# Performance work log

Hardware: AMD Instinct MI355X
Metric: run time of the kernel (lower is better)

Reference implementation:

```python
import jax, jax.numpy as jnp
import numpy as np

B, D, N_NEG, MAX_N = 4096, 256, 32768, 16
NEG_INF = float(jnp.finfo(jnp.float32).min)

def _l2norm(x):
    return x / jnp.linalg.norm(x, axis=-1, keepdims=True)

def setup_inputs() -> dict:
    key = jax.random.key(0)
    kq, kp, kn = jax.random.split(key, 3)
    q_emb = _l2norm(jax.random.normal(kq, (B, D), dtype=jnp.float32))
    p_emb = _l2norm(jax.random.normal(kp, (B, D), dtype=jnp.float32))
    n_emb = _l2norm(jax.random.normal(kn, (N_NEG, D), dtype=jnp.float32))
    # ragged counts in [0,16], mean 8, summing exactly to N_NEG
    rng = np.random.default_rng(0)
    d = rng.integers(0, 9, size=B // 2)
    counts = np.concatenate([8 + d, 8 - d])
    rng.shuffle(counts)
    n_counts = jnp.asarray(counts, dtype=jnp.int32)
    log_tau = jnp.log(jnp.asarray(0.07, dtype=jnp.float32))
    return {"q_emb": q_emb, "p_emb": p_emb, "n_emb": n_emb,
            "n_counts": n_counts, "log_tau": log_tau}

def reference(q_emb, p_emb, n_emb, n_counts, log_tau):
    Bq = q_emb.shape[0]
    tau = jnp.clip(jnp.exp(log_tau), 1e-4, 1.0)
    sim = (q_emb @ p_emb.T) / tau                      # [B, B]
    n_sim = (q_emb @ n_emb.T) / tau                    # [B, N]
    # vectorized ragged packing: query i's negatives live at
    # n_sim[i, offset[i] : offset[i]+cnt[i]]
    offsets = jnp.cumsum(n_counts) - n_counts          # [B]
    col = offsets[:, None] + jnp.arange(MAX_N)[None, :]
    valid = jnp.arange(MAX_N)[None, :] < n_counts[:, None]
    gathered = jnp.take_along_axis(n_sim, jnp.clip(col, 0, n_sim.shape[1] - 1), axis=1)
    neg_cols = jnp.where(valid, gathered, NEG_INF)     # [B, MAX_N]
    full = jnp.concatenate([sim, neg_cols], axis=1)    # [B, B+MAX_N]
    labels = jnp.arange(Bq)
    logp_q = jax.nn.log_softmax(full, axis=-1)
    loss_q = -jnp.mean(jnp.take_along_axis(logp_q, labels[:, None], axis=1))
    logp_p = jax.nn.log_softmax(sim.T, axis=-1)
    loss_p = -jnp.mean(jnp.take_along_axis(logp_p, labels[:, None], axis=1))
    return (loss_q + loss_p) / 2.0
```

## Files before the change

kernel.cpp:

```cpp
#include <hip/hip_runtime.h>
#include <math.h>

#define BQ 4096
#define DD 256
#define NNEG 32768

typedef __bf16 bf16x8 __attribute__((ext_vector_type(8)));
typedef float f32x4 __attribute__((ext_vector_type(4)));

typedef const __attribute__((address_space(1))) void GvPtr;
typedef __attribute__((address_space(3))) void LdsPtr;


__device__ __forceinline__ float get_inv_tau(const float* __restrict__ lt) {
  float tau = __expf(lt[0]);
  tau = fminf(fmaxf(tau, 1e-4f), 1.0f);
  return 1.0f / tau;
}

__device__ __forceinline__ unsigned int f2bf(float f) {
  unsigned int u = __float_as_uint(f);
  u += 0x7FFFu + ((u >> 16) & 1u);
  return u >> 16;
}

__global__ __launch_bounds__(256) void prep_kernel(
    const float* __restrict__ q, const float* __restrict__ p,
    const int* __restrict__ counts,
    ushort* __restrict__ qb, ushort* __restrict__ pb,
    int* __restrict__ owner, float* __restrict__ rowcol ) {
  __shared__ int wtot[4];
  const int t = threadIdx.x;
  if (blockIdx.x < 1024) {
    const int i = blockIdx.x * 256 + t;
    const int half = (BQ * DD) / 8;
    const float* src = (i < half) ? q : p;
    ushort* dst = (i < half) ? qb : pb;
    const int idx = (i < half) ? i : (i - half);
    const float4 a = *reinterpret_cast<const float4*>(&src[idx * 8]);
    const float4 b = *reinterpret_cast<const float4*>(&src[idx * 8 + 4]);
    uint4 o;
    o.x = f2bf(a.x) | (f2bf(a.y) << 16);
    o.y = f2bf(a.z) | (f2bf(a.w) << 16);
    o.z = f2bf(b.x) | (f2bf(b.y) << 16);
    o.w = f2bf(b.z) | (f2bf(b.w) << 16);
    *reinterpret_cast<uint4*>(&dst[idx * 8]) = o;
    return;
  }
  const int wid = t >> 6, lane = t & 63;
  const float4 z = {0.f, 0.f, 0.f, 0.f};
#pragma unroll
  for (int i = 0; i < 8; ++i) reinterpret_cast<float4*>(rowcol)[t * 8 + i] = z;

  int cl[16];
  int s = 0;
#pragma unroll
  for (int i = 0; i < 4; ++i) {
    const int4 c = reinterpret_cast<const int4*>(counts)[t * 4 + i];
    cl[4 * i + 0] = c.x; cl[4 * i + 1] = c.y; cl[4 * i + 2] = c.z; cl[4 * i + 3] = c.w;
    s += c.x + c.y + c.z + c.w;
  }
  int x = s;
#pragma unroll
  for (int off = 1; off < 64; off <<= 1) {
    const int v = __shfl_up(x, off);
    if (lane >= off) x += v;
  }
  if (lane == 63) wtot[wid] = x;
  __syncthreads();
  int base = 0;
  for (int w = 0; w < wid; ++w) base += wtot[w];
  int running = base + x - s;
#pragma unroll
  for (int k = 0; k < 16; ++k) {
    const int qi = 16 * t + k;
    for (int e = 0; e < cl[k]; ++e) owner[running + e] = qi;
    running += cl[k];
  }
}

__global__ __launch_bounds__(256) void main_kernel(
    const ushort* __restrict__ qb, const ushort* __restrict__ pb,
    const float* __restrict__ q, const float* __restrict__ n_emb,
    const int* __restrict__ owner, const float* __restrict__ logtau,
    float* __restrict__ row_sum, float* __restrict__ col_sum,
    float* __restrict__ diag) {
  __shared__ ushort As[2][128 * 32];
  __shared__ ushort Bs[2][128 * 32];

  const int tid = threadIdx.x;
  const int bid = (int)blockIdx.x;
  const float inv_tau = get_inv_tau(logtau);

  const int lane = tid & 63;
  const int wv = tid >> 6;
  const int wr = wv >> 1, wc = wv & 1;
  const int lrow = lane >> 4;
  const int lcol = lane & 15;

  const int swz = (bid & 7) * 128 + (bid >> 3);
  const int bx = swz & 31, by = swz >> 5;
  const int brow = by * 128, bcol = bx * 128;

  const int sr = tid >> 2;
  const int sc = (tid & 3) * 8;

  f32x4 acc[4][4];
#pragma unroll
  for (int i = 0; i < 4; ++i)
#pragma unroll
    for (int j = 0; j < 4; ++j) acc[i][j] = (f32x4){0.f, 0.f, 0.f, 0.f};

#define STAGE(buf, k0)                                                          \
  {                                                                             \
    _Pragma("unroll")                                                           \
    for (int i = 0; i < 2; ++i) {                                               \
      const ushort* ga = qb + (size_t)(brow + i * 64 + sr) * DD + (k0) + sc;    \
      __builtin_amdgcn_global_load_lds((GvPtr*)ga,                              \
          (LdsPtr*)(&As[buf][0] + i * 2048 + tid * 8), 16, 0, 0);               \
      const ushort* gb = pb + (size_t)(bcol + i * 64 + sr) * DD + (k0) + sc;    \
      __builtin_amdgcn_global_load_lds((GvPtr*)gb,                              \
          (LdsPtr*)(&Bs[buf][0] + i * 2048 + tid * 8), 16, 0, 0);               \
    }                                                                           \
  }

  STAGE(0, 0);
  __syncthreads();

#pragma unroll
  for (int t = 0; t < 8; ++t) {
    if (t < 7) STAGE((t + 1) & 1, (t + 1) * 32);
    const ushort* lA = &As[t & 1][0];
    const ushort* lB = &Bs[t & 1][0];
    bf16x8 a[4], b[4];
#pragma unroll
    for (int m = 0; m < 4; ++m)
      a[m] = *reinterpret_cast<const bf16x8*>(lA + (wr * 64 + m * 16 + lcol) * 32 + lrow * 8);
#pragma unroll
    for (int n = 0; n < 4; ++n)
      b[n] = *reinterpret_cast<const bf16x8*>(lB + (wc * 64 + n * 16 + lcol) * 32 + lrow * 8);
#pragma unroll
    for (int m = 0; m < 4; ++m)
#pragma unroll
      for (int n = 0; n < 4; ++n)
        acc[m][n] = __builtin_amdgcn_mfma_f32_16x16x32_bf16(a[m], b[n], acc[m][n], 0, 0, 0);
    __syncthreads();
  }
#undef STAGE

  const int arow0 = brow + wr * 64;
  const int bcol0 = bcol + wc * 64;
  float colp[4] = {0.f, 0.f, 0.f, 0.f};
#pragma unroll
  for (int mi = 0; mi < 4; ++mi) {
    float rowp[4] = {0.f, 0.f, 0.f, 0.f};
#pragma unroll
    for (int ni = 0; ni < 4; ++ni) {
      const f32x4 v = acc[mi][ni];
#pragma unroll
      for (int r = 0; r < 4; ++r) {
        const float sv = v[r] * inv_tau;
        const float e = __expf(sv);
        const int gr = arow0 + mi * 16 + lrow * 4 + r;
        const int gc = bcol0 + ni * 16 + lcol;
        if (gr == gc) diag[gr] = sv;
        rowp[r] += e;
        colp[ni] += e;
      }
    }
#pragma unroll
    for (int r = 0; r < 4; ++r) {
      float x = rowp[r];
      x += __shfl_xor(x, 1);
      x += __shfl_xor(x, 2);
      x += __shfl_xor(x, 4);
      x += __shfl_xor(x, 8);
      if (lcol == 0) atomicAdd(&row_sum[arow0 + mi * 16 + lrow * 4 + r], x);
    }
  }
#pragma unroll
  for (int ni = 0; ni < 4; ++ni) {
    float x = colp[ni];
    x += __shfl_xor(x, 16);
    x += __shfl_xor(x, 32);
    if (lrow == 0) atomicAdd(&col_sum[bcol0 + ni * 16 + lcol], x);
  }

  const int g = tid >> 3;
  const int sl = tid & 7;
  const int j = bid * 32 + g;
  const int ow = owner[j];
  const float4* nrow = reinterpret_cast<const float4*>(n_emb + (size_t)j * DD);
  const float4* qrow = reinterpret_cast<const float4*>(q + (size_t)ow * DD);
  float d0 = 0.f, d1 = 0.f;
#pragma unroll
  for (int t2 = 0; t2 < 8; t2 += 2) {
    const float4 n0 = nrow[sl + 8 * t2];
    const float4 q0 = qrow[sl + 8 * t2];
    const float4 n1 = nrow[sl + 8 * (t2 + 1)];
    const float4 q1 = qrow[sl + 8 * (t2 + 1)];
    d0 += q0.x * n0.x + q0.y * n0.y + q0.z * n0.z + q0.w * n0.w;
    d1 += q1.x * n1.x + q1.y * n1.y + q1.z * n1.z + q1.w * n1.w;
  }
  float d = d0 + d1;
  d += __shfl_xor(d, 1);
  d += __shfl_xor(d, 2);
  d += __shfl_xor(d, 4);
  if (sl == 0) atomicAdd(&row_sum[ow], __expf(d * inv_tau));
}

__global__ __launch_bounds__(1024) void finalize_kernel(
    const float* __restrict__ row_sum, const float* __restrict__ col_sum,
    const float* __restrict__ diag, float* __restrict__ out) {
  __shared__ float ws[16];
  const int t = threadIdx.x;
  const int wid = t >> 6, lane = t & 63;
  const float4 r = reinterpret_cast<const float4*>(row_sum)[t];
  const float4 c = reinterpret_cast<const float4*>(col_sum)[t];
  const float4 d = reinterpret_cast<const float4*>(diag)[t];
  float v = __logf(r.x) + __logf(r.y) + __logf(r.z) + __logf(r.w)
          + __logf(c.x) + __logf(c.y) + __logf(c.z) + __logf(c.w)
          - 2.f * (d.x + d.y + d.z + d.w);
  v += __shfl_xor(v, 1);
  v += __shfl_xor(v, 2);
  v += __shfl_xor(v, 4);
  v += __shfl_xor(v, 8);
  v += __shfl_xor(v, 16);
  v += __shfl_xor(v, 32);
  if (lane == 0) ws[wid] = v;
  __syncthreads();
  if (wid == 0) {
    float x = (lane < 16) ? ws[lane] : 0.f;
    x += __shfl_xor(x, 1);
    x += __shfl_xor(x, 2);
    x += __shfl_xor(x, 4);
    x += __shfl_xor(x, 8);
    if (lane == 0) out[0] = x / (2.0f * BQ);
  }
}

extern "C" void kernel_launch(void* const* d_in, const int* in_sizes, int n_in,
                              void* d_out, int out_size, void* d_ws, size_t ws_size,
                              hipStream_t stream) {
  const float* q      = (const float*)d_in[0];
  const float* p      = (const float*)d_in[1];
  const float* n_emb  = (const float*)d_in[2];
  const int*   counts = (const int*)d_in[3];
  const float* logtau = (const float*)d_in[4];
  float* out = (float*)d_out;

  float* ws      = (float*)d_ws;
  float* row_sum = ws;
  float* col_sum = ws + BQ;
  float* diag    = ws + 2 * BQ;
  int*   owner   = (int*)(ws + 3 * BQ);
  ushort* qb     = (ushort*)(owner + NNEG);
  ushort* pb     = qb + (size_t)BQ * DD;

  prep_kernel<<<1025, 256, 0, stream>>>(q, p, counts, qb, pb, owner, row_sum);
  main_kernel<<<1024, 256, 0, stream>>>(qb, pb, q, n_emb, owner, logtau,
                                        row_sum, col_sum, diag);
  finalize_kernel<<<1, 1024, 0, stream>>>(row_sum, col_sum, diag, out);
}
```

Measured before the change: 132.6 us.

## Use 64x64 direct-load GEMM tiles, split negatives into separate blocks, partial-sum reduction

Measured after the change: 168.9 us. +27.4%, slower.

```diff
diff --git a/kernel.cpp b/kernel.cpp
--- a/kernel.cpp
+++ b/kernel.cpp
@@ -7,9 +7,6 @@
 
 typedef __bf16 bf16x8 __attribute__((ext_vector_type(8)));
 typedef float f32x4 __attribute__((ext_vector_type(4)));
-
-typedef const __attribute__((address_space(1))) void GvPtr;
-typedef __attribute__((address_space(3))) void LdsPtr;
 
 
 __device__ __forceinline__ float get_inv_tau(const float* __restrict__ lt) {
@@ -28,7 +25,8 @@
     const float* __restrict__ q, const float* __restrict__ p,
     const int* __restrict__ counts,
     ushort* __restrict__ qb, ushort* __restrict__ pb,
-    int* __restrict__ owner, float* __restrict__ rowcol ) {
+    int* __restrict__ owner, float* __restrict__ row_acc,
+    float* __restrict__ out) {
   __shared__ int wtot[4];
   const int t = threadIdx.x;
   if (blockIdx.x < 1024) {
@@ -50,7 +48,8 @@
   const int wid = t >> 6, lane = t & 63;
   const float4 z = {0.f, 0.f, 0.f, 0.f};
 #pragma unroll
-  for (int i = 0; i < 8; ++i) reinterpret_cast<float4*>(rowcol)[t * 8 + i] = z;
+  for (int i = 0; i < 4; ++i) reinterpret_cast<float4*>(row_acc)[t * 4 + i] = z;
+  if (t == 0) out[0] = 0.f;
 
   int cl[16];
   int s = 0;
@@ -83,14 +82,40 @@
     const ushort* __restrict__ qb, const ushort* __restrict__ pb,
     const float* __restrict__ q, const float* __restrict__ n_emb,
     const int* __restrict__ owner, const float* __restrict__ logtau,
-    float* __restrict__ row_sum, float* __restrict__ col_sum,
-    float* __restrict__ diag) {
-  __shared__ ushort As[2][128 * 32];
-  __shared__ ushort Bs[2][128 * 32];
-
+    float* __restrict__ diag, float* __restrict__ row_acc,
+    float* __restrict__ rpart, float* __restrict__ cpart) {
+  __shared__ float rs[64], cs[64];
   const int tid = threadIdx.x;
   const int bid = (int)blockIdx.x;
   const float inv_tau = get_inv_tau(logtau);
+
+  if (bid < 512) {
+    const int j = bid * 64 + (tid >> 2);
+    const int sl = tid & 3;
+    const int ow = owner[j];
+    const float4* nrow = reinterpret_cast<const float4*>(n_emb + (size_t)j * DD);
+    const float4* qrow = reinterpret_cast<const float4*>(q + (size_t)ow * DD);
+    float d0 = 0.f, d1 = 0.f;
+#pragma unroll
+    for (int t2 = 0; t2 < 16; t2 += 2) {
+      const float4 n0 = nrow[sl + 4 * t2];
+      const float4 q0 = qrow[sl + 4 * t2];
+      const float4 n1 = nrow[sl + 4 * (t2 + 1)];
+      const float4 q1 = qrow[sl + 4 * (t2 + 1)];
+      d0 += q0.x * n0.x + q0.y * n0.y + q0.z * n0.z + q0.w * n0.w;
+      d1 += q1.x * n1.x + q1.y * n1.y + q1.z * n1.z + q1.w * n1.w;
+    }
+    float d = d0 + d1;
+    d += __shfl_xor(d, 1);
+    d += __shfl_xor(d, 2);
+    if (sl == 0) atomicAdd(&row_acc[ow], __expf(d * inv_tau));
+    return;
+  }
+
+  const int sb = bid - 512;
+  const int swz = (sb & 7) * 512 + (sb >> 3);
+  const int bx = swz & 63, by = swz >> 6;
+  const int brow = by * 64, bcol = bx * 64;
 
   const int lane = tid & 63;
   const int wv = tid >> 6;
@@ -98,74 +123,54 @@
   const int lrow = lane >> 4;
   const int lcol = lane & 15;
 
-  const int swz = (bid & 7) * 128 + (bid >> 3);
-  const int bx = swz & 31, by = swz >> 5;
-  const int brow = by * 128, bcol = bx * 128;
-
-  const int sr = tid >> 2;
-  const int sc = (tid & 3) * 8;
-
-  f32x4 acc[4][4];
-#pragma unroll
-  for (int i = 0; i < 4; ++i)
-#pragma unroll
-    for (int j = 0; j < 4; ++j) acc[i][j] = (f32x4){0.f, 0.f, 0.f, 0.f};
-
-#define STAGE(buf, k0)                                                          \
-  {                                                                             \
-    _Pragma("unroll")                                                           \
-    for (int i = 0; i < 2; ++i) {                                               \
-      const ushort* ga = qb + (size_t)(brow + i * 64 + sr) * DD + (k0) + sc;    \
-      __builtin_amdgcn_global_load_lds((GvPtr*)ga,                              \
-          (LdsPtr*)(&As[buf][0] + i * 2048 + tid * 8), 16, 0, 0);               \
-      const ushort* gb = pb + (size_t)(bcol + i * 64 + sr) * DD + (k0) + sc;    \
-      __builtin_amdgcn_global_load_lds((GvPtr*)gb,                              \
-          (LdsPtr*)(&Bs[buf][0] + i * 2048 + tid * 8), 16, 0, 0);               \
-    }                                                                           \
-  }
-
-  STAGE(0, 0);
-  __syncthreads();
-
-#pragma unroll
-  for (int t = 0; t < 8; ++t) {
-    if (t < 7) STAGE((t + 1) & 1, (t + 1) * 32);
-    const ushort* lA = &As[t & 1][0];
-    const ushort* lB = &Bs[t & 1][0];
-    bf16x8 a[4], b[4];
-#pragma unroll
-    for (int m = 0; m < 4; ++m)
-      a[m] = *reinterpret_cast<const bf16x8*>(lA + (wr * 64 + m * 16 + lcol) * 32 + lrow * 8);
-#pragma unroll
-    for (int n = 0; n < 4; ++n)
-      b[n] = *reinterpret_cast<const bf16x8*>(lB + (wc * 64 + n * 16 + lcol) * 32 + lrow * 8);
-#pragma unroll
-    for (int m = 0; m < 4; ++m)
-#pragma unroll
-      for (int n = 0; n < 4; ++n)
-        acc[m][n] = __builtin_amdgcn_mfma_f32_16x16x32_bf16(a[m], b[n], acc[m][n], 0, 0, 0);
-    __syncthreads();
-  }
-#undef STAGE
-
-  const int arow0 = brow + wr * 64;
-  const int bcol0 = bcol + wc * 64;
-  float colp[4] = {0.f, 0.f, 0.f, 0.f};
-#pragma unroll
-  for (int mi = 0; mi < 4; ++mi) {
+  if (tid < 64) { rs[tid] = 0.f; cs[tid] = 0.f; }
+
+  const ushort* ab = qb + (size_t)(brow + wr * 32 + lcol) * DD + lrow * 8;
+  const ushort* bb = pb + (size_t)(bcol + wc * 32 + lcol) * DD + lrow * 8;
+
+  f32x4 acc[2][2];
+#pragma unroll
+  for (int m = 0; m < 2; ++m)
+#pragma unroll
+    for (int n = 0; n < 2; ++n) acc[m][n] = (f32x4){0.f, 0.f, 0.f, 0.f};
+
+#pragma unroll
+  for (int k0 = 0; k0 < DD; k0 += 64) {
+    bf16x8 a[2][2], b[2][2];
+#pragma unroll
+    for (int s = 0; s < 2; ++s)
+#pragma unroll
+      for (int m = 0; m < 2; ++m) {
+        a[s][m] = *reinterpret_cast<const bf16x8*>(ab + (size_t)m * 16 * DD + k0 + s * 32);
+        b[s][m] = *reinterpret_cast<const bf16x8*>(bb + (size_t)m * 16 * DD + k0 + s * 32);
+      }
+#pragma unroll
+    for (int s = 0; s < 2; ++s)
+#pragma unroll
+      for (int m = 0; m < 2; ++m)
+#pragma unroll
+        for (int n = 0; n < 2; ++n)
+          acc[m][n] = __builtin_amdgcn_mfma_f32_16x16x32_bf16(a[s][m], b[s][n], acc[m][n], 0, 0, 0);
+  }
+
+  __syncthreads();
+
+  float colp[2] = {0.f, 0.f};
+#pragma unroll
+  for (int m = 0; m < 2; ++m) {
     float rowp[4] = {0.f, 0.f, 0.f, 0.f};
 #pragma unroll
-    for (int ni = 0; ni < 4; ++ni) {
-      const f32x4 v = acc[mi][ni];
+    for (int n = 0; n < 2; ++n) {
+      const f32x4 v = acc[m][n];
 #pragma unroll
       for (int r = 0; r < 4; ++r) {
         const float sv = v[r] * inv_tau;
         const float e = __expf(sv);
-        const int gr = arow0 + mi * 16 + lrow * 4 + r;
-        const int gc = bcol0 + ni * 16 + lcol;
+        const int gr = brow + wr * 32 + m * 16 + lrow * 4 + r;
+        const int gc = bcol + wc * 32 + n * 16 + lcol;
         if (gr == gc) diag[gr] = sv;
         rowp[r] += e;
-        colp[ni] += e;
+        colp[n] += e;
       }
     }
 #pragma unroll
@@ -175,67 +180,51 @@
       x += __shfl_xor(x, 2);
       x += __shfl_xor(x, 4);
       x += __shfl_xor(x, 8);
-      if (lcol == 0) atomicAdd(&row_sum[arow0 + mi * 16 + lrow * 4 + r], x);
+      if (lcol == 0) atomicAdd(&rs[wr * 32 + m * 16 + lrow * 4 + r], x);
     }
   }
 #pragma unroll
-  for (int ni = 0; ni < 4; ++ni) {
-    float x = colp[ni];
+  for (int n = 0; n < 2; ++n) {
+    float x = colp[n];
     x += __shfl_xor(x, 16);
     x += __shfl_xor(x, 32);
-    if (lrow == 0) atomicAdd(&col_sum[bcol0 + ni * 16 + lcol], x);
-  }
-
-  const int g = tid >> 3;
-  const int sl = tid & 7;
-  const int j = bid * 32 + g;
-  const int ow = owner[j];
-  const float4* nrow = reinterpret_cast<const float4*>(n_emb + (size_t)j * DD);
-  const float4* qrow = reinterpret_cast<const float4*>(q + (size_t)ow * DD);
-  float d0 = 0.f, d1 = 0.f;
-#pragma unroll
-  for (int t2 = 0; t2 < 8; t2 += 2) {
-    const float4 n0 = nrow[sl + 8 * t2];
-    const float4 q0 = qrow[sl + 8 * t2];
-    const float4 n1 = nrow[sl + 8 * (t2 + 1)];
-    const float4 q1 = qrow[sl + 8 * (t2 + 1)];
-    d0 += q0.x * n0.x + q0.y * n0.y + q0.z * n0.z + q0.w * n0.w;
-    d1 += q1.x * n1.x + q1.y * n1.y + q1.z * n1.z + q1.w * n1.w;
-  }
-  float d = d0 + d1;
-  d += __shfl_xor(d, 1);
-  d += __shfl_xor(d, 2);
-  d += __shfl_xor(d, 4);
-  if (sl == 0) atomicAdd(&row_sum[ow], __expf(d * inv_tau));
-}
-
-__global__ __launch_bounds__(1024) void finalize_kernel(
-    const float* __restrict__ row_sum, const float* __restrict__ col_sum,
-    const float* __restrict__ diag, float* __restrict__ out) {
-  __shared__ float ws[16];
-  const int t = threadIdx.x;
-  const int wid = t >> 6, lane = t & 63;
-  const float4 r = reinterpret_cast<const float4*>(row_sum)[t];
-  const float4 c = reinterpret_cast<const float4*>(col_sum)[t];
-  const float4 d = reinterpret_cast<const float4*>(diag)[t];
-  float v = __logf(r.x) + __logf(r.y) + __logf(r.z) + __logf(r.w)
-          + __logf(c.x) + __logf(c.y) + __logf(c.z) + __logf(c.w)
-          - 2.f * (d.x + d.y + d.z + d.w);
-  v += __shfl_xor(v, 1);
-  v += __shfl_xor(v, 2);
-  v += __shfl_xor(v, 4);
-  v += __shfl_xor(v, 8);
-  v += __shfl_xor(v, 16);
-  v += __shfl_xor(v, 32);
-  if (lane == 0) ws[wid] = v;
-  __syncthreads();
-  if (wid == 0) {
-    float x = (lane < 16) ? ws[lane] : 0.f;
-    x += __shfl_xor(x, 1);
-    x += __shfl_xor(x, 2);
-    x += __shfl_xor(x, 4);
-    x += __shfl_xor(x, 8);
-    if (lane == 0) out[0] = x / (2.0f * BQ);
+    if (lrow == 0) atomicAdd(&cs[wc * 32 + n * 16 + lcol], x);
+  }
+  __syncthreads();
+  if (tid < 64) {
+    rpart[(size_t)bx * BQ + brow + tid] = rs[tid];
+    cpart[(size_t)by * BQ + bcol + tid] = cs[tid];
+  }
+}
+
+__global__ __launch_bounds__(256) void fin_kernel(
+    const float* __restrict__ diag, const float* __restrict__ row_acc,
+    const float* __restrict__ rpart, const float* __restrict__ cpart,
+    float* __restrict__ out) {
+  __shared__ float R[4][64], C[4][64];
+  const int k = (int)blockIdx.x, tid = threadIdx.x;
+  const int r = tid & 63, w = tid >> 6;
+  const int i = k * 64 + r;
+  float rt = 0.f, ct = 0.f;
+#pragma unroll 4
+  for (int t = w; t < 64; t += 4) {
+    rt += rpart[(size_t)t * BQ + i];
+    ct += cpart[(size_t)t * BQ + i];
+  }
+  R[w][r] = rt;
+  C[w][r] = ct;
+  __syncthreads();
+  if (tid < 64) {
+    const float row_tot = R[0][tid] + R[1][tid] + R[2][tid] + R[3][tid] + row_acc[k * 64 + tid];
+    const float col_tot = C[0][tid] + C[1][tid] + C[2][tid] + C[3][tid];
+    float v = __logf(row_tot) + __logf(col_tot) - 2.f * diag[k * 64 + tid];
+    v += __shfl_xor(v, 1);
+    v += __shfl_xor(v, 2);
+    v += __shfl_xor(v, 4);
+    v += __shfl_xor(v, 8);
+    v += __shfl_xor(v, 16);
+    v += __shfl_xor(v, 32);
+    if (tid == 0) atomicAdd(out, v * (1.f / (2.f * BQ)));
   }
 }
 
@@ -250,15 +239,16 @@
   float* out = (float*)d_out;
 
   float* ws      = (float*)d_ws;
-  float* row_sum = ws;
-  float* col_sum = ws + BQ;
-  float* diag    = ws + 2 * BQ;
-  int*   owner   = (int*)(ws + 3 * BQ);
+  float* diag    = ws;
+  float* row_acc = ws + BQ;
+  float* rpart   = ws + 2 * BQ;
+  float* cpart   = rpart + 64 * BQ;
+  int*   owner   = (int*)(cpart + 64 * BQ);
   ushort* qb     = (ushort*)(owner + NNEG);
   ushort* pb     = qb + (size_t)BQ * DD;
 
-  prep_kernel<<<1025, 256, 0, stream>>>(q, p, counts, qb, pb, owner, row_sum);
-  main_kernel<<<1024, 256, 0, stream>>>(qb, pb, q, n_emb, owner, logtau,
-                                        row_sum, col_sum, diag);
-  finalize_kernel<<<1, 1024, 0, stream>>>(row_sum, col_sum, diag, out);
-}
+  prep_kernel<<<1025, 256, 0, stream>>>(q, p, counts, qb, pb, owner, row_acc, out);
+  main_kernel<<<512 + 4096, 256, 0, stream>>>(qb, pb, q, n_emb, owner, logtau,
+                                              diag, row_acc, rpart, cpart);
+  fin_kernel<<<64, 256, 0, stream>>>(diag, row_acc, rpart, cpart, out);
+}
```
